# Performance work log

Measured on AMD Instinct MI355X. Metric: run time of the kernel, lower is better.

Reference implementation:

```python
import jax, jax.numpy as jnp
import numpy as np

# Module constants derived from default grid_config
D = 59          # depth bins: (60-1)/1
C_OUT = 64
X, Y, Z = 128, 128, 7
STRIDE = 16
GRID_LB = np.array([-51.2, -51.2, -2.5], dtype=np.float32)
GRID_IV = np.array([0.8, 0.8, 1.0], dtype=np.float32)
D0, DSTEP = 1.0, 1.0

B, N, C_IN, H, W = 4, 6, 256, 16, 44


def _voxel_coords():
    xs, ys, zs = np.meshgrid(np.arange(X), np.arange(Y), np.arange(Z), indexing='ij')
    coords = np.stack([xs, ys, zs], axis=-1).reshape(-1, 3).astype(np.float32)
    coords = coords * GRID_IV + GRID_LB  # [V, 3] ego-frame voxel centers
    return coords


def _camera_rig(rng):
    """Realistic 6-camera rig: yawed cameras looking outward, z_cam = forward."""
    c2e = np.zeros((B, N, 4, 4), dtype=np.float32)
    K = np.zeros((B, N, 3, 3), dtype=np.float32)
    for b in range(B):
        for n in range(N):
            a = 2.0 * np.pi * n / N + 0.02 * rng.standard_normal()
            f = np.array([np.cos(a), np.sin(a), 0.0])           # camera forward (z_cam)
            x_cam = np.array([-np.sin(a), np.cos(a), 0.0])      # camera right
            y_cam = np.array([0.0, 0.0, -1.0])                   # camera down
            R = np.stack([x_cam, y_cam, f], axis=1)              # columns = cam axes in ego
            t = 1.0 * f + np.array([0.0, 0.0, 1.5])
            c2e[b, n, :3, :3] = R
            c2e[b, n, :3, 3] = t
            c2e[b, n, 3, 3] = 1.0
            fl = 400.0 + 5.0 * rng.standard_normal()
            K[b, n] = np.array([[fl, 0.0, 352.0], [0.0, fl, 128.0], [0.0, 0.0, 1.0]])
    return c2e, K


def setup_inputs() -> dict:
    key = jax.random.key(0)
    k1, k2, k3 = jax.random.split(key, 3)
    img_feats = jax.random.normal(k1, (B, N, C_IN, H, W), dtype=jnp.float32)
    c2e, K = _camera_rig(np.random.default_rng(0))
    # depth_net: 1x1 conv in_channels -> D + C_OUT
    w_depth = jax.random.normal(k2, (D + C_OUT, C_IN), dtype=jnp.float32) * (1.0 / np.sqrt(C_IN))
    b_depth = jax.random.normal(k3, (D + C_OUT,), dtype=jnp.float32) * 0.01
    return {
        'img_feats': img_feats,
        'cam2ego': jnp.asarray(c2e),
        'cam_intrinsics': jnp.asarray(K),
        'w_depth': w_depth,
        'b_depth': b_depth,
    }


def reference(img_feats, cam2ego, cam_intrinsics, w_depth, b_depth):
    Bc, Nc, C, Hc, Wc = img_feats.shape
    # 1x1 conv == per-pixel linear
    x = jnp.einsum('bnchw,oc->bnhwo', img_feats, w_depth) + b_depth  # [B,N,H,W,D+C_OUT]
    depth = jax.nn.softmax(x[..., :D], axis=-1)                      # [B,N,H,W,D]
    feat = x[..., D:]                                                # [B,N,H,W,C_OUT]

    vox = jnp.asarray(_voxel_coords())                               # [V,3]
    V = vox.shape[0]
    vox_h = jnp.concatenate([vox, jnp.ones((V, 1), vox.dtype)], axis=1)  # [V,4]

    e2c = jnp.linalg.inv(cam2ego)                                    # [B,N,4,4]
    cam = jnp.einsum('bnij,vj->bnvi', e2c, vox_h)[..., :3]           # [B,N,V,3]
    z = cam[..., 2]
    z_safe = jnp.maximum(z, 0.1)
    norm = cam[..., :2] / z_safe[..., None]
    homo = jnp.concatenate([norm, jnp.ones_like(z[..., None])], axis=-1)  # [B,N,V,3]
    img = jnp.einsum('bnij,bnvj->bnvi', cam_intrinsics, homo)[..., :2]
    fc = img / STRIDE                                                # feature-plane coords

    depth_bin = ((z - D0) / DSTEP).astype(jnp.int32)                 # trunc toward 0, matches .long()
    valid = (
        (fc[..., 0] >= 0) & (fc[..., 0] < Wc)
        & (fc[..., 1] >= 0) & (fc[..., 1] < Hc)
        & (z > 0.5)
        & (depth_bin >= 0) & (depth_bin < D)
    )

    u = jnp.clip(fc[..., 0].astype(jnp.int32), 0, Wc - 1)            # [B,N,V]
    v = jnp.clip(fc[..., 1].astype(jnp.int32), 0, Hc - 1)
    d = jnp.clip(depth_bin, 0, D - 1)
    hw = v * Wc + u

    feat_flat = feat.reshape(Bc, Nc, Hc * Wc, C_OUT)
    sampled_feat = jnp.take_along_axis(feat_flat, hw[..., None], axis=2)   # [B,N,V,C_OUT]
    depth_flat = depth.reshape(Bc, Nc, Hc * Wc * D)
    sampled_depth = jnp.take_along_axis(depth_flat, hw * D + d, axis=2)    # [B,N,V]

    wgt = sampled_depth * valid.astype(sampled_depth.dtype)
    # scatter_add at flat_idx == voxel index (identity) -> masked sum over cameras
    bev = jnp.einsum('bnv,bnvc->bvc', wgt, sampled_feat)             # [B,V,C_OUT]
    bev = bev.reshape(Bc, X, Y, Z, C_OUT).sum(axis=3)                # collapse Z
    bev = bev.transpose(0, 3, 2, 1)                                  # [B,C_OUT,Y,X]
    return bev, depth
```

## Files before the change

### kernel.cpp

```cpp
#include <hip/hip_runtime.h>
#include <math.h>

#define D_BINS 59
#define CO     64
#define CI     256
#define NB     4
#define NC     6
#define H_IMG  16
#define W_IMG  44
#define HW     704
#define NPIX   (NB*NC*HW)
#define XD     128
#define YD     128
#define ZD     7
#define NOUT   123
#define PXB    66

__device__ void inv_rigid(const float* __restrict__ M, float* __restrict__ o) {
    double a = M[0], b = M[1], c = M[2], t0 = M[3];
    double d = M[4], e = M[5], f = M[6], t1 = M[7];
    double g = M[8], h = M[9], ii = M[10], t2 = M[11];
    double A00 = e*ii - f*h, A01 = c*h - b*ii, A02 = b*f - c*e;
    double A10 = f*g - d*ii, A11 = a*ii - c*g, A12 = c*d - a*f;
    double A20 = d*h - e*g,  A21 = b*g - a*h,  A22 = a*e - b*d;
    double det = a*A00 + b*A10 + c*A20;
    double inv = 1.0 / det;
    double r00 = A00*inv, r01 = A01*inv, r02 = A02*inv;
    double r10 = A10*inv, r11 = A11*inv, r12 = A12*inv;
    double r20 = A20*inv, r21 = A21*inv, r22 = A22*inv;
    o[0] = (float)r00; o[1] = (float)r01; o[2]  = (float)r02;
    o[3] = (float)(-(r00*t0 + r01*t1 + r02*t2));
    o[4] = (float)r10; o[5] = (float)r11; o[6]  = (float)r12;
    o[7] = (float)(-(r10*t0 + r11*t1 + r12*t2));
    o[8] = (float)r20; o[9] = (float)r21; o[10] = (float)r22;
    o[11] = (float)(-(r20*t0 + r21*t1 + r22*t2));
}

__global__ __launch_bounds__(256) void k_pre(
    const float* __restrict__ wd, const float* __restrict__ c2e,
    float* __restrict__ wt, float* __restrict__ e2c) {
    const int o = blockIdx.x;
    const int k = threadIdx.x;
    float v = (o < NOUT) ? wd[(size_t)o * CI + k] : 0.f;
    wt[(size_t)k * 128 + o] = v;
    if (blockIdx.x == 0 && k < NB * NC)
        inv_rigid(c2e + k * 16, e2c + k * 12);
}

__global__ __launch_bounds__(640) void k_head(
    const float* __restrict__ img, const float* __restrict__ wt,
    const float* __restrict__ bd, float* __restrict__ depth_out,
    float* __restrict__ feat_ws) {
    __shared__ float smem[PXB * 132 + PXB];
    float* S = smem + PXB * 132;

    const int tid = threadIdx.x;
    const int wv  = tid >> 6;
    const int ln  = tid & 63;
    const int p0  = blockIdx.x * PXB;
    const bool is_main = (wv < 8);
    const int o0  = __builtin_amdgcn_readfirstlane((is_main ? wv : 0) << 4);
    const int epx = 64 + (wv - 8);

    float acc[16];
#pragma unroll
    for (int j = 0; j < 16; ++j) acc[j] = 0.f;
    float acc2[2] = {0.f, 0.f};

    for (int kc = 0; kc < 4; ++kc) {
#pragma unroll
        for (int it = 0; it < 7; ++it) {
            int idx = tid + it * 640;
            if (idx < 64 * PXB) {
                int kl = idx / PXB, px = idx - kl * PXB;
                int p = p0 + px;
                int bn = p / HW, hw = p - bn * HW;
                smem[kl * PXB + px] =
                    img[((size_t)bn * CI + kc * 64 + kl) * HW + hw];
            }
        }
        __syncthreads();
        if (is_main) {
            const float* wr = wt + (size_t)(kc * 64) * 128 + o0;
#pragma unroll 4
            for (int k = 0; k < 64; ++k) {
                float a = smem[k * PXB + ln];
                const float* w = wr + k * 128;
#pragma unroll
                for (int j = 0; j < 16; ++j)
                    acc[j] = fmaf(a, w[j], acc[j]);
            }
        } else {
#pragma unroll 4
            for (int k = 0; k < 64; ++k) {
                float a = smem[k * PXB + epx];
                const float* w = wt + (size_t)(kc * 64 + k) * 128;
                acc2[0] = fmaf(a, w[ln], acc2[0]);
                acc2[1] = fmaf(a, w[ln + 64], acc2[1]);
            }
        }
        __syncthreads();
    }

    float* X = smem;
    if (is_main) {
#pragma unroll
        for (int j = 0; j < 16; ++j) {
            int o = o0 + j;
            if (o < NOUT) {
                int col = (o < D_BINS) ? o : o + 5;
                X[ln * 132 + col] = acc[j] + bd[o];
            }
        }
    } else {
        int o = ln;
        X[epx * 132 + ((o < D_BINS) ? o : o + 5)] = acc2[0] + bd[o];
        o = ln + 64;
        if (o < NOUT)
            X[epx * 132 + ((o < D_BINS) ? o : o + 5)] = acc2[1] + bd[o];
    }
    __syncthreads();

#pragma unroll
    for (int it = 0; it < 2; ++it) {
        int g = tid + it * 640;
        if (g < PXB * 16) {
            int p = g >> 4, m = g & 15;
            float4 v = *(const float4*)(X + p * 132 + 64 + m * 4);
            *(float4*)(feat_ws + (size_t)(p0 + p) * CO + m * 4) = v;
        }
    }

    if (tid < PXB) {
        float* row = X + tid * 132;
        float m = row[0];
        for (int o = 1; o < D_BINS; ++o) m = fmaxf(m, row[o]);
        float s = 0.f;
        for (int o = 0; o < D_BINS; ++o) {
            float e = __expf(row[o] - m);
            row[o] = e;
            s += e;
        }
        S[tid] = 1.f / s;
    }
    __syncthreads();

    for (int g = tid; g < PXB * D_BINS; g += 640) {
        int p = g / D_BINS;
        int o = g - p * D_BINS;
        depth_out[(size_t)p0 * D_BINS + g] = X[p * 132 + o] * S[p];
    }
}

__global__ __launch_bounds__(256) void k_splat(
    const float* __restrict__ e2c, const float* __restrict__ Kmat,
    const float* __restrict__ depth_g, const float* __restrict__ feat_ws,
    float* __restrict__ bev) {
    const int tx   = threadIdx.x;
    const int half = threadIdx.y & 1;
    const int yq   = threadIdx.y >> 1;
    const int x = blockIdx.x * 64 + tx;
    const int y = blockIdx.y * 2 + yq;
    const int b = blockIdx.z;
    const float wx = (float)x * 0.8f + (-51.2f);
    const float wy = (float)y * 0.8f + (-51.2f);

    float acc[32];
#pragma unroll
    for (int m = 0; m < 32; ++m) acc[m] = 0.f;

    for (int n = 0; n < NC; ++n) {
        const int bn = b * NC + n;
        const float* E = e2c + bn * 12;
        const float* Km = Kmat + bn * 9;
        const float k00 = Km[0], k01 = Km[1], k02 = Km[2];
        const float k10 = Km[3], k11 = Km[4], k12 = Km[5];
        const float e02 = E[2], e12 = E[6], e22 = E[10];
        const float bx0 = E[0] * wx + E[1] * wy + E[3];
        const float bx1 = E[4] * wx + E[5] * wy + E[7];
        const float bx2 = E[8] * wx + E[9] * wy + E[11];
#pragma unroll
        for (int z = 0; z < ZD; ++z) {
            const float wz = -2.5f + (float)z;
            const float cx = bx0 + e02 * wz;
            const float cy = bx1 + e12 * wz;
            const float cz = bx2 + e22 * wz;
            const float zs = fmaxf(cz, 0.1f);
            const float rz = 1.0f / zs;
            const float xn = cx * rz;
            const float yn = cy * rz;
            const float fu = (k00 * xn + k01 * yn + k02) * 0.0625f;
            const float fv = (k10 * xn + k11 * yn + k12) * 0.0625f;
            const int bin = (int)(cz - 1.0f);
            const bool valid = (fu >= 0.f) & (fu < (float)W_IMG) &
                               (fv >= 0.f) & (fv < (float)H_IMG) &
                               (cz > 0.5f) & (bin >= 0) & (bin < D_BINS);
            if (valid) {
                int u = (int)fu;
                int v = (int)fv;
                int hw = v * W_IMG + u;
                float wgt = depth_g[((size_t)bn * HW + hw) * D_BINS + bin];
                const float4* fp =
                    (const float4*)(feat_ws + ((size_t)bn * HW + hw) * CO + half * 32);
#pragma unroll
                for (int q = 0; q < 8; ++q) {
                    float4 f = fp[q];
                    acc[q * 4 + 0] = fmaf(wgt, f.x, acc[q * 4 + 0]);
                    acc[q * 4 + 1] = fmaf(wgt, f.y, acc[q * 4 + 1]);
                    acc[q * 4 + 2] = fmaf(wgt, f.z, acc[q * 4 + 2]);
                    acc[q * 4 + 3] = fmaf(wgt, f.w, acc[q * 4 + 3]);
                }
            }
        }
    }
    float* ob = bev + (((size_t)b * CO + half * 32) * YD + y) * XD + x;
#pragma unroll
    for (int m = 0; m < 32; ++m) ob[(size_t)m * YD * XD] = acc[m];
}

extern "C" void kernel_launch(void* const* d_in, const int* in_sizes, int n_in,
                              void* d_out, int out_size, void* d_ws, size_t ws_size,
                              hipStream_t stream) {
    const float* img  = (const float*)d_in[0];
    const float* c2e  = (const float*)d_in[1];
    const float* Kmat = (const float*)d_in[2];
    const float* wd   = (const float*)d_in[3];
    const float* bd   = (const float*)d_in[4];
    float* bev = (float*)d_out;
    float* depth_out = bev + (size_t)NB * CO * YD * XD;
    float* feat_ws = (float*)d_ws;
    float* wt  = feat_ws + (size_t)NPIX * CO;
    float* e2c = wt + 256 * 128;

    k_pre<<<128, 256, 0, stream>>>(wd, c2e, wt, e2c);
    k_head<<<256, 640, 0, stream>>>(img, wt, bd, depth_out, feat_ws);
    k_splat<<<dim3(2, 64, NB), dim3(64, 4, 1), 0, stream>>>(e2c, Kmat, depth_out,
                                                            feat_ws, bev);
}
```

Measured before the change: 132.1 us.

## Pack k-pairs for packed FMA in head GEMM and split splat channels four ways

The head GEMM weight and shared-memory image layouts are interleaved in k pairs, so each thread can use two-wide vector FMAs (which can map to packed FP32 FMA on CDNA). The two partial sums are added at the end. The splat kernel now gives each thread 16 channels instead of 32, with four channel groups per pixel row and twice as many blocks. This lowers register pressure and raises occupancy, at the cost of repeating the projection and depth gather four times per voxel instead of twice.

```diff
diff --git a/kernel.cpp b/kernel.cpp
--- a/kernel.cpp
+++ b/kernel.cpp
@@ -15,6 +15,8 @@
 #define ZD     7
 #define NOUT   123
 #define PXB    66
+
+typedef float v2f __attribute__((ext_vector_type(2)));
 
 __device__ void inv_rigid(const float* __restrict__ M, float* __restrict__ o) {
     double a = M[0], b = M[1], c = M[2], t0 = M[3];
@@ -38,17 +40,17 @@
 
 __global__ __launch_bounds__(256) void k_pre(
     const float* __restrict__ wd, const float* __restrict__ c2e,
-    float* __restrict__ wt, float* __restrict__ e2c) {
+    float* __restrict__ wt2, float* __restrict__ e2c) {
     const int o = blockIdx.x;
     const int k = threadIdx.x;
     float v = (o < NOUT) ? wd[(size_t)o * CI + k] : 0.f;
-    wt[(size_t)k * 128 + o] = v;
+    wt2[(size_t)(k >> 1) * 256 + o * 2 + (k & 1)] = v;
     if (blockIdx.x == 0 && k < NB * NC)
         inv_rigid(c2e + k * 16, e2c + k * 12);
 }
 
 __global__ __launch_bounds__(640) void k_head(
-    const float* __restrict__ img, const float* __restrict__ wt,
+    const float* __restrict__ img, const float* __restrict__ wt2,
     const float* __restrict__ bd, float* __restrict__ depth_out,
     float* __restrict__ feat_ws) {
     __shared__ float smem[PXB * 132 + PXB];
@@ -62,10 +64,10 @@
     const int o0  = __builtin_amdgcn_readfirstlane((is_main ? wv : 0) << 4);
     const int epx = 64 + (wv - 8);
 
-    float acc[16];
-#pragma unroll
-    for (int j = 0; j < 16; ++j) acc[j] = 0.f;
-    float acc2[2] = {0.f, 0.f};
+    v2f acc[16];
+#pragma unroll
+    for (int j = 0; j < 16; ++j) acc[j] = (v2f)(0.f);
+    v2f acc2a = (v2f)(0.f), acc2b = (v2f)(0.f);
 
     for (int kc = 0; kc < 4; ++kc) {
 #pragma unroll
@@ -75,28 +77,30 @@
                 int kl = idx / PXB, px = idx - kl * PXB;
                 int p = p0 + px;
                 int bn = p / HW, hw = p - bn * HW;
-                smem[kl * PXB + px] =
+                smem[(kl >> 1) * 132 + px * 2 + (kl & 1)] =
                     img[((size_t)bn * CI + kc * 64 + kl) * HW + hw];
             }
         }
         __syncthreads();
         if (is_main) {
-            const float* wr = wt + (size_t)(kc * 64) * 128 + o0;
 #pragma unroll 4
-            for (int k = 0; k < 64; ++k) {
-                float a = smem[k * PXB + ln];
-                const float* w = wr + k * 128;
+            for (int k2 = 0; k2 < 32; ++k2) {
+                v2f a = *(const v2f*)(smem + k2 * 132 + ln * 2);
+                const v2f* w =
+                    (const v2f*)(wt2 + (size_t)(kc * 32 + k2) * 256) + o0;
 #pragma unroll
                 for (int j = 0; j < 16; ++j)
-                    acc[j] = fmaf(a, w[j], acc[j]);
+                    acc[j] = __builtin_elementwise_fma(a, w[j], acc[j]);
             }
         } else {
 #pragma unroll 4
-            for (int k = 0; k < 64; ++k) {
-                float a = smem[k * PXB + epx];
-                const float* w = wt + (size_t)(kc * 64 + k) * 128;
-                acc2[0] = fmaf(a, w[ln], acc2[0]);
-                acc2[1] = fmaf(a, w[ln + 64], acc2[1]);
+            for (int k2 = 0; k2 < 32; ++k2) {
+                v2f a = *(const v2f*)(smem + k2 * 132 + epx * 2);
+                const float* w = wt2 + (size_t)(kc * 32 + k2) * 256;
+                v2f w0 = {w[ln * 2], w[ln * 2 + 1]};
+                v2f w1 = {w[(ln + 64) * 2], w[(ln + 64) * 2 + 1]};
+                acc2a = __builtin_elementwise_fma(a, w0, acc2a);
+                acc2b = __builtin_elementwise_fma(a, w1, acc2b);
             }
         }
         __syncthreads();
@@ -109,15 +113,15 @@
             int o = o0 + j;
             if (o < NOUT) {
                 int col = (o < D_BINS) ? o : o + 5;
-                X[ln * 132 + col] = acc[j] + bd[o];
+                X[ln * 132 + col] = (acc[j].x + acc[j].y) + bd[o];
             }
         }
     } else {
         int o = ln;
-        X[epx * 132 + ((o < D_BINS) ? o : o + 5)] = acc2[0] + bd[o];
+        X[epx * 132 + ((o < D_BINS) ? o : o + 5)] = (acc2a.x + acc2a.y) + bd[o];
         o = ln + 64;
         if (o < NOUT)
-            X[epx * 132 + ((o < D_BINS) ? o : o + 5)] = acc2[1] + bd[o];
+            X[epx * 132 + ((o < D_BINS) ? o : o + 5)] = (acc2b.x + acc2b.y) + bd[o];
     }
     __syncthreads();
 
@@ -156,18 +160,17 @@
     const float* __restrict__ e2c, const float* __restrict__ Kmat,
     const float* __restrict__ depth_g, const float* __restrict__ feat_ws,
     float* __restrict__ bev) {
-    const int tx   = threadIdx.x;
-    const int half = threadIdx.y & 1;
-    const int yq   = threadIdx.y >> 1;
+    const int tx = threadIdx.x;
+    const int cq = threadIdx.y;
     const int x = blockIdx.x * 64 + tx;
-    const int y = blockIdx.y * 2 + yq;
+    const int y = blockIdx.y;
     const int b = blockIdx.z;
     const float wx = (float)x * 0.8f + (-51.2f);
     const float wy = (float)y * 0.8f + (-51.2f);
 
-    float acc[32];
-#pragma unroll
-    for (int m = 0; m < 32; ++m) acc[m] = 0.f;
+    float acc[16];
+#pragma unroll
+    for (int m = 0; m < 16; ++m) acc[m] = 0.f;
 
     for (int n = 0; n < NC; ++n) {
         const int bn = b * NC + n;
@@ -201,21 +204,30 @@
                 int hw = v * W_IMG + u;
                 float wgt = depth_g[((size_t)bn * HW + hw) * D_BINS + bin];
                 const float4* fp =
-                    (const float4*)(feat_ws + ((size_t)bn * HW + hw) * CO + half * 32);
-#pragma unroll
-                for (int q = 0; q < 8; ++q) {
-                    float4 f = fp[q];
-                    acc[q * 4 + 0] = fmaf(wgt, f.x, acc[q * 4 + 0]);
-                    acc[q * 4 + 1] = fmaf(wgt, f.y, acc[q * 4 + 1]);
-                    acc[q * 4 + 2] = fmaf(wgt, f.z, acc[q * 4 + 2]);
-                    acc[q * 4 + 3] = fmaf(wgt, f.w, acc[q * 4 + 3]);
-                }
-            }
-        }
-    }
-    float* ob = bev + (((size_t)b * CO + half * 32) * YD + y) * XD + x;
-#pragma unroll
-    for (int m = 0; m < 32; ++m) ob[(size_t)m * YD * XD] = acc[m];
+                    (const float4*)(feat_ws + ((size_t)bn * HW + hw) * CO + cq * 16);
+                float4 f0 = fp[0], f1 = fp[1], f2 = fp[2], f3 = fp[3];
+                acc[0]  = fmaf(wgt, f0.x, acc[0]);
+                acc[1]  = fmaf(wgt, f0.y, acc[1]);
+                acc[2]  = fmaf(wgt, f0.z, acc[2]);
+                acc[3]  = fmaf(wgt, f0.w, acc[3]);
+                acc[4]  = fmaf(wgt, f1.x, acc[4]);
+                acc[5]  = fmaf(wgt, f1.y, acc[5]);
+                acc[6]  = fmaf(wgt, f1.z, acc[6]);
+                acc[7]  = fmaf(wgt, f1.w, acc[7]);
+                acc[8]  = fmaf(wgt, f2.x, acc[8]);
+                acc[9]  = fmaf(wgt, f2.y, acc[9]);
+                acc[10] = fmaf(wgt, f2.z, acc[10]);
+                acc[11] = fmaf(wgt, f2.w, acc[11]);
+                acc[12] = fmaf(wgt, f3.x, acc[12]);
+                acc[13] = fmaf(wgt, f3.y, acc[13]);
+                acc[14] = fmaf(wgt, f3.z, acc[14]);
+                acc[15] = fmaf(wgt, f3.w, acc[15]);
+            }
+        }
+    }
+    float* ob = bev + (((size_t)b * CO + cq * 16) * YD + y) * XD + x;
+#pragma unroll
+    for (int m = 0; m < 16; ++m) ob[(size_t)m * YD * XD] = acc[m];
 }
 
 extern "C" void kernel_launch(void* const* d_in, const int* in_sizes, int n_in,
@@ -229,11 +241,11 @@
     float* bev = (float*)d_out;
     float* depth_out = bev + (size_t)NB * CO * YD * XD;
     float* feat_ws = (float*)d_ws;
-    float* wt  = feat_ws + (size_t)NPIX * CO;
-    float* e2c = wt + 256 * 128;
-
-    k_pre<<<128, 256, 0, stream>>>(wd, c2e, wt, e2c);
-    k_head<<<256, 640, 0, stream>>>(img, wt, bd, depth_out, feat_ws);
-    k_splat<<<dim3(2, 64, NB), dim3(64, 4, 1), 0, stream>>>(e2c, Kmat, depth_out,
+    float* wt2 = feat_ws + (size_t)NPIX * CO;
+    float* e2c = wt2 + 128 * 256;
+
+    k_pre<<<128, 256, 0, stream>>>(wd, c2e, wt2, e2c);
+    k_head<<<256, 640, 0, stream>>>(img, wt2, bd, depth_out, feat_ws);
+    k_splat<<<dim3(2, YD, NB), dim3(64, 4, 1), 0, stream>>>(e2c, Kmat, depth_out,
                                                             feat_ws, bev);
 }
```

New measurement: 126.3 us. -4.4%, faster.
